# Performance work log

Hardware: AMD Instinct MI355X
Metric: run time of the kernel (lower is better)

The kernel has to match this reference:

```python
import jax, jax.numpy as jnp
import numpy as np

GX, GY = 512, 512   # grid_size
MAX_PT = 64         # max_pt_per_encode


def setup_inputs() -> dict:
    key = jax.random.key(0)
    k1, k2 = jax.random.split(key)
    B, N = 16, 262144
    pt_fea = jax.random.normal(k1, (B, N, 4), dtype=jnp.float32)
    xy_ind = jax.random.randint(k2, (B, N, 2), 0, GX, dtype=jnp.int32)
    return {"pt_fea": pt_fea, "xy_ind": xy_ind}


def _voxelize(fea, vid, P, S):
    # fea: [P,4] flat point features; vid: [P] linearized (batch,x,y) voxel id.
    # --- 'random' point selection: keep first MAX_PT points per voxel ---
    order = jnp.argsort(vid)                       # stable sort -> group points by voxel
    svid = vid[order]
    ar = jnp.arange(P, dtype=jnp.int32)
    change = jnp.concatenate([jnp.ones((1,), dtype=bool), svid[1:] != svid[:-1]])
    start = jax.lax.cummax(jnp.where(change, ar, 0))  # first sorted-index of each group
    rank_sorted = ar - start                          # within-group rank (grp_range_torch)
    grp_ind = jnp.zeros(P, jnp.int32).at[order].set(rank_sorted)
    remain = grp_ind < MAX_PT
    # --- scatter_max pooling of z; gather r at argmax; clamped counts ---
    z = jnp.where(remain, fea[:, 2], -jnp.inf)
    h = jax.ops.segment_max(z, vid, num_segments=S)
    cnt = jax.ops.segment_sum(remain.astype(jnp.float32), vid, num_segments=S)  # == clamp(count, max_pt)
    occ = cnt > 0
    cand = jnp.where(remain & (fea[:, 2] == h[vid]), ar, P)  # argmax via min index of max match
    argm = jax.ops.segment_min(cand, vid, num_segments=S)
    r = jnp.where(occ, fea[jnp.minimum(argm, P - 1), 3], 0.0)
    h0 = jnp.where(occ, h, 0.0)  # empty voxels stay 0 (dense zeros grid write)
    return h0, r, cnt


def reference(pt_fea, xy_ind):
    B, N, _ = pt_fea.shape
    P = B * N
    S = B * GX * GY
    fea = pt_fea.reshape(P, 4)
    b = jnp.repeat(jnp.arange(B, dtype=jnp.int32), N)
    x = xy_ind[..., 0].reshape(P).astype(jnp.int32)
    y = xy_ind[..., 1].reshape(P).astype(jnp.int32)
    vid = (b * GX + x) * GY + y
    h0, r, cnt = _voxelize(fea, vid, P, S)
    grid = jnp.stack([h0, r, cnt], axis=-1).reshape(B, GX, GY, 3)
    grid = jnp.transpose(grid, (0, 3, 1, 2))  # [B, 3, GX, GY]
    mx = grid.max(axis=(2, 3), keepdims=True)
    mn = grid.min(axis=(2, 3), keepdims=True)
    return (grid - mn) / (mx - mn)
```

## Files before the change

kernel.cpp:

```cpp
#include <hip/hip_runtime.h>
#include <stdint.h>

#define GXC 512
#define GYC 512
#define GXY (GXC * GYC)
#define NB  512
#define SC  8192
#define PT  1024
#define SPT (SC / PT)
#define LBINS 512
#define XG  4
#define BPB (GXY / 256)

typedef float v4f __attribute__((ext_vector_type(4)));
typedef int   v2i __attribute__((ext_vector_type(2)));

__device__ __forceinline__ unsigned f2s(float f) {
    unsigned u = __float_as_uint(f);
    return (u & 0x80000000u) ? ~u : (u | 0x80000000u);
}
__device__ __forceinline__ float s2f(unsigned u) {
    return (u & 0x80000000u) ? __uint_as_float(u ^ 0x80000000u)
                             : __uint_as_float(~u);
}
__device__ __forceinline__ unsigned long long packkey_y(float z, float r,
                                                        unsigned y) {
    return ((unsigned long long)f2s(z) << 32)
         | (unsigned long long)((f2s(r) & ~511u) | y);
}
__device__ __forceinline__ unsigned long long packkey(float z, float r) {
    return ((unsigned long long)f2s(z) << 32) | (unsigned long long)f2s(r);
}

__device__ __forceinline__ int swizzle(int g, int swz) {
    return swz ? ((g & 7) * (NB / 8) + (g >> 3)) : g;
}


__global__ __launch_bounds__(1024)
void place_kernel(const v4f* __restrict__ fea, const v2i* __restrict__ xy,
                  unsigned long long* __restrict__ keyA,
                  unsigned* __restrict__ meta, int swz) {
    __shared__ unsigned long long skey[SC];
    __shared__ unsigned lcnt[LBINS], loff[LBINS];
    __shared__ unsigned wsum[8];
    int t = threadIdx.x;
    int blk = swizzle(blockIdx.x, swz);
    int start = blk * SC;
    if (t < LBINS) lcnt[t] = 0;
    __syncthreads();

    unsigned long long k[SPT]; unsigned lb[SPT], rk[SPT];
    #pragma unroll
    for (int kk = 0; kk < SPT; ++kk) {
        int p = start + t + kk * PT;
        v2i q = __builtin_nontemporal_load(xy + p);
        v4f ff = __builtin_nontemporal_load(fea + p);
        k[kk]  = packkey_y(ff.z, ff.w, (unsigned)q.y);
        lb[kk] = (unsigned)q.x;
        rk[kk] = atomicAdd(&lcnt[q.x], 1u);
    }
    __syncthreads();

    unsigned c = 0, inc = 0;
    if (t < LBINS) {
        c = lcnt[t];
        inc = c;
        int lane = t & 63;
        #pragma unroll
        for (int off = 1; off < 64; off <<= 1) {
            unsigned o = __shfl_up(inc, off);
            if (lane >= off) inc += o;
        }
        if (lane == 63) wsum[t >> 6] = inc;
    }
    __syncthreads();
    if (t < 8) {
        unsigned v = wsum[t], i2 = v;
        #pragma unroll
        for (int off = 1; off < 8; off <<= 1) {
            unsigned o = __shfl_up(i2, off, 8);
            if (t >= off) i2 += o;
        }
        wsum[t] = i2 - v;
    }
    __syncthreads();
    if (t < LBINS) loff[t] = inc - c + wsum[t >> 6];
    __syncthreads();

    #pragma unroll
    for (int kk = 0; kk < SPT; ++kk)
        skey[loff[lb[kk]] + rk[kk]] = k[kk];
    __syncthreads();

    unsigned long long* dst = keyA + (size_t)blk * SC;
    #pragma unroll
    for (int kk = 0; kk < SPT; ++kk) {
        int s = t + kk * PT;
        dst[s] = skey[s];
    }
    if (t < LBINS)
        meta[(size_t)blk * LBINS + t] = (loff[t] << 16) | lcnt[t];
}

__global__ __launch_bounds__(512)
void rowreduce_kernel(const unsigned long long* __restrict__ keyA,
                      const unsigned* __restrict__ meta,
                      float* __restrict__ out,
                      float* __restrict__ partials,
                      int bpblk) {
    __shared__ unsigned long long sk[XG * 512];
    __shared__ unsigned scnt[XG * 512];
    __shared__ float red[8][6];
    int t = threadIdx.x;
    int g = blockIdx.x;
    int batch = g >> 7;
    int xg = g & 127;
    int x0 = xg * XG;
    for (int i = t; i < XG * 512; i += 512) { sk[i] = 0; scnt[i] = 0; }
    __syncthreads();

    int seg = t >> 4, l16 = t & 15;
    size_t sidx = (size_t)(batch * bpblk + seg);
    uint4 m = *(const uint4*)(meta + sidx * LBINS + x0);
    unsigned lo0 = m.x >> 16;
    unsigned b1 = m.x & 0xFFFFu;
    unsigned b2 = b1 + (m.y & 0xFFFFu);
    unsigned b3 = b2 + (m.z & 0xFFFFu);
    unsigned tot = b3 + (m.w & 0xFFFFu);
    const unsigned long long* src = keyA + sidx * SC + lo0;
    for (unsigned r = l16; r < tot; r += 16) {
        unsigned long long k = src[r];
        int bin = (r >= b1) + (r >= b2) + (r >= b3);
        unsigned y = (unsigned)k & 511u;
        atomicMax(&sk[(bin << 9) + y], k);
        atomicAdd(&scnt[(bin << 9) + y], 1u);
    }
    __syncthreads();

    size_t ob = ((size_t)batch * 3) << 18;
    size_t xoff = (size_t)x0 << 9;
    float n0 = INFINITY, mx0 = -INFINITY, n1 = INFINITY, mx1 = -INFINITY,
          n2 = INFINITY, mx2 = -INFINITY;
    for (int i = t; i < XG * 512; i += 512) {
        unsigned cv = scnt[i];
        float h0 = 0.0f, r = 0.0f;
        if (cv) {
            unsigned long long k = sk[i];
            h0 = s2f((unsigned)(k >> 32));
            r  = s2f((unsigned)k & ~511u);
        }
        float cf = (float)cv;
        out[ob + xoff + i] = h0;
        out[ob + (size_t)GXY + xoff + i] = r;
        out[ob + (size_t)(2 * GXY) + xoff + i] = cf;
        n0 = fminf(n0, h0); mx0 = fmaxf(mx0, h0);
        n1 = fminf(n1, r);  mx1 = fmaxf(mx1, r);
        n2 = fminf(n2, cf); mx2 = fmaxf(mx2, cf);
    }
    #pragma unroll
    for (int off = 32; off; off >>= 1) {
        n0 = fminf(n0, __shfl_down(n0, off));  mx0 = fmaxf(mx0, __shfl_down(mx0, off));
        n1 = fminf(n1, __shfl_down(n1, off));  mx1 = fmaxf(mx1, __shfl_down(mx1, off));
        n2 = fminf(n2, __shfl_down(n2, off));  mx2 = fmaxf(mx2, __shfl_down(mx2, off));
    }
    int lane = t & 63, wave = t >> 6;
    if (lane == 0) {
        red[wave][0] = n0; red[wave][1] = mx0;
        red[wave][2] = n1; red[wave][3] = mx1;
        red[wave][4] = n2; red[wave][5] = mx2;
    }
    __syncthreads();
    if (t < 6) {
        int j = t;
        float v = red[0][j];
        bool isMin = (j & 1) == 0;
        #pragma unroll
        for (int w = 1; w < 8; ++w)
            v = isMin ? fminf(v, red[w][j]) : fmaxf(v, red[w][j]);
        partials[(size_t)g * 6 + j] = v;
    }
}

__global__ void reduce_kernel(const float* __restrict__ partials,
                              float* __restrict__ mn,
                              float* __restrict__ mx,
                              int rows) {
    int b = blockIdx.x / 6;
    int j = blockIdx.x - b * 6;
    bool isMin = (j & 1) == 0;
    float v = isMin ? INFINITY : -INFINITY;
    for (int i = threadIdx.x; i < rows; i += blockDim.x) {
        float p = partials[((size_t)b * rows + i) * 6 + j];
        v = isMin ? fminf(v, p) : fmaxf(v, p);
    }
    #pragma unroll
    for (int off = 32; off; off >>= 1) {
        float o = __shfl_down(v, off);
        v = isMin ? fminf(v, o) : fmaxf(v, o);
    }
    __shared__ float red[4];
    int lane = threadIdx.x & 63, wave = threadIdx.x >> 6;
    if (lane == 0) red[wave] = v;
    __syncthreads();
    if (threadIdx.x == 0) {
        #pragma unroll
        for (int w = 1; w < 4 && w < (int)(blockDim.x >> 6); ++w)
            v = isMin ? fminf(v, red[w]) : fmaxf(v, red[w]);
        int slot = b * 3 + (j >> 1);
        if (isMin) mn[slot] = v; else mx[slot] = v;
    }
}

__global__ void norm_kernel(v4f* __restrict__ out,
                            const float* __restrict__ mn,
                            const float* __restrict__ mx,
                            int total4) {
    int i = blockIdx.x * blockDim.x + threadIdx.x;
    if (i >= total4) return;
    int slot = i >> 16;
    float lo = mn[slot];
    float inv = 1.0f / (mx[slot] - lo);
    v4f v = __builtin_nontemporal_load(out + i);
    v.x = (v.x - lo) * inv;
    v.y = (v.y - lo) * inv;
    v.z = (v.z - lo) * inv;
    v.w = (v.w - lo) * inv;
    __builtin_nontemporal_store(v, out + i);
}

__global__ void scatter_fb(const v4f* __restrict__ fea, const v2i* __restrict__ xy,
                           unsigned long long* __restrict__ keys,
                           unsigned* __restrict__ cnt32, int N, int P) {
    int p = blockIdx.x * blockDim.x + threadIdx.x;
    if (p >= P) return;
    v2i q = __builtin_nontemporal_load(xy + p);
    v4f f = __builtin_nontemporal_load(fea + p);
    int vid = ((p / N) * GXC + q.x) * GYC + q.y;
    atomicMax(&keys[vid], packkey(f.z, f.w));
    atomicAdd(&cnt32[vid >> 2], 1u << ((vid & 3) * 8));
}

__global__ void fill_fb(const unsigned long long* __restrict__ keys,
                        const unsigned char* __restrict__ cntB,
                        float* __restrict__ out, float* __restrict__ partials) {
    int g = blockIdx.x;
    int batch = g / BPB, blkInB = g - batch * BPB;
    int rem = blkInB * 256 + threadIdx.x;
    int s = batch * GXY + rem;
    unsigned c = cntB[s];
    float h0 = 0.0f, r = 0.0f;
    if (c) {
        unsigned long long k = keys[s];
        h0 = s2f((unsigned)(k >> 32));
        r  = s2f((unsigned)(k & 0xFFFFFFFFull));
    }
    float cf = (float)c;
    size_t base = (size_t)batch * 3 * GXY + rem;
    out[base] = h0; out[base + GXY] = r; out[base + 2 * GXY] = cf;
    float n0 = h0, x0 = h0, n1 = r, x1 = r, n2 = cf, x2 = cf;
    #pragma unroll
    for (int off = 32; off; off >>= 1) {
        n0 = fminf(n0, __shfl_down(n0, off)); x0 = fmaxf(x0, __shfl_down(x0, off));
        n1 = fminf(n1, __shfl_down(n1, off)); x1 = fmaxf(x1, __shfl_down(x1, off));
        n2 = fminf(n2, __shfl_down(n2, off)); x2 = fmaxf(x2, __shfl_down(x2, off));
    }
    __shared__ float red[4][6];
    int lane = threadIdx.x & 63, wave = threadIdx.x >> 6;
    if (lane == 0) {
        red[wave][0] = n0; red[wave][1] = x0; red[wave][2] = n1;
        red[wave][3] = x1; red[wave][4] = n2; red[wave][5] = x2;
    }
    __syncthreads();
    if (threadIdx.x < 6) {
        int j = threadIdx.x;
        float v = red[0][j];
        bool isMin = (j & 1) == 0;
        #pragma unroll
        for (int w = 1; w < 4; ++w)
            v = isMin ? fminf(v, red[w][j]) : fmaxf(v, red[w][j]);
        partials[(size_t)(batch * BPB + blkInB) * 6 + j] = v;
    }
}

extern "C" void kernel_launch(void* const* d_in, const int* in_sizes, int n_in,
                              void* d_out, int out_size, void* d_ws, size_t ws_size,
                              hipStream_t stream) {
    const v4f* fea = (const v4f*)d_in[0];
    const v2i* xy  = (const v2i*)d_in[1];

    int P = in_sizes[0] / 4;
    int B = out_size / (3 * GXY);
    int N = (B > 0) ? P / B : 0;
    int S = B * GXY;
    int NBIN = B * GXC;
    int bpblk = (B > 0) ? NB / B : 0;

    char* ws = (char*)d_ws;
    unsigned long long* keyA = (unsigned long long*)ws;
    size_t o = (size_t)P * 8;
    unsigned* meta = (unsigned*)(ws + o);   o += (size_t)NB * LBINS * 4;
    float* partials = (float*)(ws + o);     o += (size_t)(NBIN / XG) * 6 * 4;
    float* mn = (float*)(ws + o);           o += (size_t)B * 3 * 4;
    float* mx = (float*)(ws + o);           o += (size_t)B * 3 * 4;
    size_t need = o;

    int swz = (B % 8 == 0) ? 1 : 0;

    bool ok = B > 0 && NB % B == 0 && bpblk == 32 && P == NB * SC
              && N == bpblk * SC && ws_size >= need;

    if (ok) {
        place_kernel<<<NB, PT, 0, stream>>>(fea, xy, keyA, meta, swz);
        rowreduce_kernel<<<NBIN / XG, 512, 0, stream>>>(keyA, meta,
                                                        (float*)d_out, partials,
                                                        bpblk);
        reduce_kernel<<<B * 6, 256, 0, stream>>>(partials, mn, mx, GXC / XG);
    } else {
        float* mn_f = (float*)ws;
        float* mx_f = (float*)(ws + 256);
        float* part_f = (float*)(ws + 512);
        size_t hdr = 512 + (size_t)B * BPB * 6 * 4;
        unsigned long long* keys = (unsigned long long*)(ws + hdr);
        unsigned char* cntB = (unsigned char*)(ws + hdr + (size_t)S * 8);
        mn = mn_f; mx = mx_f;
        (void)hipMemsetAsync(keys, 0x00, (size_t)S * 9, stream);
        scatter_fb<<<(P + 255) / 256, 256, 0, stream>>>(fea, xy, keys,
                                                        (unsigned*)cntB, N, P);
        fill_fb<<<S / 256, 256, 0, stream>>>(keys, cntB, (float*)d_out, part_f);
        reduce_kernel<<<B * 6, 256, 0, stream>>>(part_f, mn_f, mx_f, BPB);
    }
    norm_kernel<<<(out_size / 4 + 255) / 256, 256, 0, stream>>>((v4f*)d_out,
                                                                mn, mx, out_size / 4);
}
```

Measured before the change: 166.6 us.

## Fuse row reduction, min/max reduce and normalization into one cooperative kernel

Replaces the rowreduce, reduce and norm kernels with a single cooperative kernel that builds a 16-row voxel tile in shared memory, computes per-block min/max, and uses two grid-wide syncs to finish the per-batch reduction. It then writes the normalized output directly with nontemporal stores. This avoids writing the unnormalized grid and reading it back, and removes two launches. Counts are packed as bytes in shared memory so the larger tile fits, and the place kernel now loads only the z/r pair instead of the full float4. Risks: grid.sync overhead, only 512 blocks with large LDS limiting occupancy, and byte counters that overflow if a voxel receives more than 255 points from one block.

After: 255.2 us. 1.53x slower.

```diff
diff --git a/kernel.cpp b/kernel.cpp
--- a/kernel.cpp
+++ b/kernel.cpp
@@ -1,5 +1,8 @@
 #include <hip/hip_runtime.h>
+#include <hip/hip_cooperative_groups.h>
 #include <stdint.h>
+
+namespace cg = cooperative_groups;
 
 #define GXC 512
 #define GYC 512
@@ -10,9 +13,11 @@
 #define SPT (SC / PT)
 #define LBINS 512
 #define XG  4
+#define XG2 16
 #define BPB (GXY / 256)
 
 typedef float v4f __attribute__((ext_vector_type(4)));
+typedef float v2f __attribute__((ext_vector_type(2)));
 typedef int   v2i __attribute__((ext_vector_type(2)));
 
 __device__ __forceinline__ unsigned f2s(float f) {
@@ -36,9 +41,8 @@
     return swz ? ((g & 7) * (NB / 8) + (g >> 3)) : g;
 }
 
-
 __global__ __launch_bounds__(1024)
-void place_kernel(const v4f* __restrict__ fea, const v2i* __restrict__ xy,
+void place_kernel(const v2f* __restrict__ zr, const v2i* __restrict__ xy,
                   unsigned long long* __restrict__ keyA,
                   unsigned* __restrict__ meta, int swz) {
     __shared__ unsigned long long skey[SC];
@@ -55,8 +59,8 @@
     for (int kk = 0; kk < SPT; ++kk) {
         int p = start + t + kk * PT;
         v2i q = __builtin_nontemporal_load(xy + p);
-        v4f ff = __builtin_nontemporal_load(fea + p);
-        k[kk]  = packkey_y(ff.z, ff.w, (unsigned)q.y);
+        v2f f = __builtin_nontemporal_load(zr + 2 * p + 1);
+        k[kk]  = packkey_y(f.x, f.y, (unsigned)q.y);
         lb[kk] = (unsigned)q.x;
         rk[kk] = atomicAdd(&lcnt[q.x], 1u);
     }
@@ -101,6 +105,128 @@
     }
     if (t < LBINS)
         meta[(size_t)blk * LBINS + t] = (loff[t] << 16) | lcnt[t];
+}
+
+__global__ __launch_bounds__(512)
+void fused_kernel(const unsigned long long* __restrict__ keyA,
+                  const unsigned* __restrict__ meta,
+                  float* __restrict__ out,
+                  float* __restrict__ partials,
+                  float* __restrict__ mnmx,
+                  int bpblk, int B) {
+    __shared__ unsigned long long sk[XG2 * 512];
+    __shared__ unsigned scnt32[(XG2 * 512) / 4];
+    __shared__ unsigned short bnd[32][XG2 + 1];
+    __shared__ unsigned slo[32];
+    __shared__ float red[8][6];
+    cg::grid_group grid = cg::this_grid();
+    int t = threadIdx.x;
+    int g = blockIdx.x;
+    int batch = g >> 5;
+    int x0 = (g & 31) * XG2;
+
+    for (int i = t; i < XG2 * 512; i += 512) sk[i] = 0;
+    for (int i = t; i < (XG2 * 512) / 4; i += 512) scnt32[i] = 0;
+
+    int seg = t >> 4, l16 = t & 15;
+    size_t sidx = (size_t)(batch * bpblk + seg);
+    unsigned m = meta[sidx * LBINS + x0 + l16];
+    unsigned pc = m & 0xFFFFu, ip = pc;
+    #pragma unroll
+    for (int off = 1; off < 16; off <<= 1) {
+        unsigned o = __shfl_up(ip, off, 16);
+        if (l16 >= off) ip += o;
+    }
+    bnd[seg][l16 + 1] = (unsigned short)ip;
+    if (l16 == 0) { bnd[seg][0] = 0; slo[seg] = m >> 16; }
+    __syncthreads();
+
+    unsigned tot = bnd[seg][XG2];
+    const unsigned long long* src = keyA + sidx * SC + slo[seg];
+    unsigned b = 0;
+    for (unsigned r = l16; r < tot; r += 16) {
+        while (r >= bnd[seg][b + 1]) ++b;
+        unsigned long long k = src[r];
+        unsigned idx = (b << 9) | ((unsigned)k & 511u);
+        atomicMax(&sk[idx], k);
+        atomicAdd(&scnt32[idx >> 2], 1u << ((idx & 3) * 8));
+    }
+    __syncthreads();
+
+    float n0 = INFINITY, mx0 = -INFINITY, n1 = INFINITY, mx1 = -INFINITY,
+          n2 = INFINITY, mx2 = -INFINITY;
+    for (int i = t; i < XG2 * 512; i += 512) {
+        unsigned cv = (scnt32[i >> 2] >> ((i & 3) * 8)) & 255u;
+        float h0 = 0.0f, r = 0.0f;
+        if (cv) {
+            unsigned long long k = sk[i];
+            h0 = s2f((unsigned)(k >> 32));
+            r  = s2f((unsigned)k & ~511u);
+        }
+        float cf = (float)cv;
+        n0 = fminf(n0, h0); mx0 = fmaxf(mx0, h0);
+        n1 = fminf(n1, r);  mx1 = fmaxf(mx1, r);
+        n2 = fminf(n2, cf); mx2 = fmaxf(mx2, cf);
+    }
+    #pragma unroll
+    for (int off = 32; off; off >>= 1) {
+        n0 = fminf(n0, __shfl_down(n0, off));  mx0 = fmaxf(mx0, __shfl_down(mx0, off));
+        n1 = fminf(n1, __shfl_down(n1, off));  mx1 = fmaxf(mx1, __shfl_down(mx1, off));
+        n2 = fminf(n2, __shfl_down(n2, off));  mx2 = fmaxf(mx2, __shfl_down(mx2, off));
+    }
+    int lane = t & 63, wave = t >> 6;
+    if (lane == 0) {
+        red[wave][0] = n0; red[wave][1] = mx0;
+        red[wave][2] = n1; red[wave][3] = mx1;
+        red[wave][4] = n2; red[wave][5] = mx2;
+    }
+    __syncthreads();
+    if (t < 6) {
+        float v = red[0][t];
+        bool isMin = (t & 1) == 0;
+        #pragma unroll
+        for (int w = 1; w < 8; ++w)
+            v = isMin ? fminf(v, red[w][t]) : fmaxf(v, red[w][t]);
+        partials[(size_t)g * 6 + t] = v;
+    }
+    grid.sync();
+
+    if (g < B * 6) {
+        int bb = g / 6, j = g - bb * 6;
+        bool isMin = (j & 1) == 0;
+        if (t < 32) {
+            float v = partials[(size_t)(bb * 32 + t) * 6 + j];
+            #pragma unroll
+            for (int off = 16; off; off >>= 1) {
+                float o = __shfl_down(v, off, 32);
+                v = isMin ? fminf(v, o) : fmaxf(v, o);
+            }
+            if (t == 0) {
+                int slot = bb * 3 + (j >> 1);
+                mnmx[(isMin ? 0 : 3 * B) + slot] = v;
+            }
+        }
+    }
+    grid.sync();
+
+    float lo0 = mnmx[batch * 3 + 0], iv0 = 1.0f / (mnmx[3 * B + batch * 3 + 0] - lo0);
+    float lo1 = mnmx[batch * 3 + 1], iv1 = 1.0f / (mnmx[3 * B + batch * 3 + 1] - lo1);
+    float lo2 = mnmx[batch * 3 + 2], iv2 = 1.0f / (mnmx[3 * B + batch * 3 + 2] - lo2);
+    size_t ob = ((size_t)batch * 3) << 18;
+    size_t xoff = (size_t)x0 << 9;
+    for (int i = t; i < XG2 * 512; i += 512) {
+        unsigned cv = (scnt32[i >> 2] >> ((i & 3) * 8)) & 255u;
+        float h0 = 0.0f, r = 0.0f;
+        if (cv) {
+            unsigned long long k = sk[i];
+            h0 = s2f((unsigned)(k >> 32));
+            r  = s2f((unsigned)k & ~511u);
+        }
+        float cf = (float)cv;
+        __builtin_nontemporal_store((h0 - lo0) * iv0, out + ob + xoff + i);
+        __builtin_nontemporal_store((r  - lo1) * iv1, out + ob + (size_t)GXY + xoff + i);
+        __builtin_nontemporal_store((cf - lo2) * iv2, out + ob + (size_t)(2 * GXY) + xoff + i);
+    }
 }
 
 __global__ __launch_bounds__(512)
@@ -115,11 +241,9 @@
     int t = threadIdx.x;
     int g = blockIdx.x;
     int batch = g >> 7;
-    int xg = g & 127;
-    int x0 = xg * XG;
+    int x0 = (g & 127) * XG;
     for (int i = t; i < XG * 512; i += 512) { sk[i] = 0; scnt[i] = 0; }
     __syncthreads();
-
     int seg = t >> 4, l16 = t & 15;
     size_t sidx = (size_t)(batch * bpblk + seg);
     uint4 m = *(const uint4*)(meta + sidx * LBINS + x0);
@@ -137,7 +261,6 @@
         atomicAdd(&scnt[(bin << 9) + y], 1u);
     }
     __syncthreads();
-
     size_t ob = ((size_t)batch * 3) << 18;
     size_t xoff = (size_t)x0 << 9;
     float n0 = INFINITY, mx0 = -INFINITY, n1 = INFINITY, mx1 = -INFINITY,
@@ -172,13 +295,12 @@
     }
     __syncthreads();
     if (t < 6) {
-        int j = t;
-        float v = red[0][j];
-        bool isMin = (j & 1) == 0;
+        float v = red[0][t];
+        bool isMin = (t & 1) == 0;
         #pragma unroll
         for (int w = 1; w < 8; ++w)
-            v = isMin ? fminf(v, red[w][j]) : fmaxf(v, red[w][j]);
-        partials[(size_t)g * 6 + j] = v;
+            v = isMin ? fminf(v, red[w][t]) : fmaxf(v, red[w][t]);
+        partials[(size_t)g * 6 + t] = v;
     }
 }
 
@@ -308,14 +430,24 @@
     int swz = (B % 8 == 0) ? 1 : 0;
 
     bool ok = B > 0 && NB % B == 0 && bpblk == 32 && P == NB * SC
-              && N == bpblk * SC && ws_size >= need;
+              && N == bpblk * SC && GXC / XG2 == 32 && ws_size >= need;
 
     if (ok) {
-        place_kernel<<<NB, PT, 0, stream>>>(fea, xy, keyA, meta, swz);
-        rowreduce_kernel<<<NBIN / XG, 512, 0, stream>>>(keyA, meta,
-                                                        (float*)d_out, partials,
-                                                        bpblk);
-        reduce_kernel<<<B * 6, 256, 0, stream>>>(partials, mn, mx, GXC / XG);
+        place_kernel<<<NB, PT, 0, stream>>>((const v2f*)fea, xy, keyA, meta, swz);
+        int grid2 = B * (GXC / XG2);
+        void* args[] = { (void*)&keyA, (void*)&meta, (void*)&d_out,
+                         (void*)&partials, (void*)&mn, (void*)&bpblk, (void*)&B };
+        hipError_t ce = hipLaunchCooperativeKernel((const void*)fused_kernel,
+                                                   dim3(grid2), dim3(512),
+                                                   args, 0, stream);
+        if (ce != hipSuccess) {
+            rowreduce_kernel<<<NBIN / XG, 512, 0, stream>>>(keyA, meta,
+                                                            (float*)d_out,
+                                                            partials, bpblk);
+            reduce_kernel<<<B * 6, 256, 0, stream>>>(partials, mn, mx, GXC / XG);
+            norm_kernel<<<(out_size / 4 + 255) / 256, 256, 0, stream>>>(
+                (v4f*)d_out, mn, mx, out_size / 4);
+        }
     } else {
         float* mn_f = (float*)ws;
         float* mx_f = (float*)(ws + 256);
@@ -323,13 +455,12 @@
         size_t hdr = 512 + (size_t)B * BPB * 6 * 4;
         unsigned long long* keys = (unsigned long long*)(ws + hdr);
         unsigned char* cntB = (unsigned char*)(ws + hdr + (size_t)S * 8);
-        mn = mn_f; mx = mx_f;
         (void)hipMemsetAsync(keys, 0x00, (size_t)S * 9, stream);
         scatter_fb<<<(P + 255) / 256, 256, 0, stream>>>(fea, xy, keys,
                                                         (unsigned*)cntB, N, P);
         fill_fb<<<S / 256, 256, 0, stream>>>(keys, cntB, (float*)d_out, part_f);
         reduce_kernel<<<B * 6, 256, 0, stream>>>(part_f, mn_f, mx_f, BPB);
-    }
-    norm_kernel<<<(out_size / 4 + 255) / 256, 256, 0, stream>>>((v4f*)d_out,
-                                                                mn, mx, out_size / 4);
-}
+        norm_kernel<<<(out_size / 4 + 255) / 256, 256, 0, stream>>>(
+            (v4f*)d_out, mn_f, mx_f, out_size / 4);
+    }
+}
```
